# Optimization experiments

Hardware: AMD Instinct MI355X
Metric: run time of the kernel (lower is better)

Reference implementation:

```python
import jax, jax.numpy as jnp
import numpy as np

N, E, IN, HID, H, G, OUT = 50000, 800000, 128, 96, 8, 64, 10
D = HID // H  # per-head dim = 12


def setup_inputs() -> dict:
    key = jax.random.key(0)
    ks = jax.random.split(key, 24)
    s = 0.1
    inp = {
        'x': jax.random.normal(ks[0], (N, IN), jnp.float32),
        'src': jax.random.randint(ks[1], (E,), 0, N, jnp.int32),
        'dst': jax.random.randint(ks[2], (E,), 0, N, jnp.int32),
        'graph_id': jax.random.randint(ks[3], (N,), 0, G, jnp.int32),
        # GraphConv layers (norm='both', weight + bias)
        'W1': jax.random.normal(ks[4], (IN, HID), jnp.float32) * s,
        'b1': jnp.zeros((HID,), jnp.float32),
        'W2': jax.random.normal(ks[5], (HID, HID), jnp.float32) * s,
        'b2': jnp.zeros((HID,), jnp.float32),
        # 3 GATv2 layers, stacked params
        'Ws': jax.random.normal(ks[6], (3, HID, HID), jnp.float32) * s,
        'bs': jnp.zeros((3, HID), jnp.float32),
        'Wd': jax.random.normal(ks[7], (3, HID, HID), jnp.float32) * s,
        'bd': jnp.zeros((3, HID), jnp.float32),
        'attn': jax.random.normal(ks[8], (3, H, D), jnp.float32) * s,
        # classifier MLP (dropout is identity at inference)
        'Wc1': jax.random.normal(ks[9], (HID, HID), jnp.float32) * s,
        'bc1': jnp.zeros((HID,), jnp.float32),
        'Wc2': jax.random.normal(ks[10], (HID, HID // 2), jnp.float32) * s,
        'bc2': jnp.zeros((HID // 2,), jnp.float32),
        'Wc3': jax.random.normal(ks[11], (HID // 2, OUT), jnp.float32) * s,
        'bc3': jnp.zeros((OUT,), jnp.float32),
    }
    return inp


def _graph_conv(h, W, b, src, dst):
    # DGL GraphConv, norm='both', allow_zero_in_degree (degrees clamped to >=1)
    ones = jnp.ones((E,), h.dtype)
    deg_out = jnp.clip(jax.ops.segment_sum(ones, src, N), 1.0)
    deg_in = jnp.clip(jax.ops.segment_sum(ones, dst, N), 1.0)
    h = (h * (deg_out ** -0.5)[:, None]) @ W          # [N, out]
    agg = jax.ops.segment_sum(h[src], dst, N)          # sum over in-edges
    return agg * (deg_in ** -0.5)[:, None] + b


def _gatv2(h, Ws, bs, Wd, bd, attn, src, dst):
    fs = (h @ Ws + bs).reshape(N, H, D)
    fd = (h @ Wd + bd).reshape(N, H, D)
    e = jax.nn.leaky_relu(fs[src] + fd[dst], 0.2)      # [E, H, D]
    logits = jnp.einsum('ehd,hd->eh', e, attn)         # [E, H]
    # edge softmax over incoming edges of each dst node
    m = jax.ops.segment_max(logits, dst, N)            # [N, H]
    ex = jnp.exp(logits - m[dst])
    den = jax.ops.segment_sum(ex, dst, N)              # [N, H]
    a = ex / den[dst]                                  # [E, H]
    rst = jax.ops.segment_sum(a[:, :, None] * fs[src], dst, N)  # [N, H, D]
    return jax.nn.relu(rst).reshape(N, HID)            # activation=relu, then view


def reference(x, src, dst, graph_id, W1, b1, W2, b2, Ws, bs, Wd, bd, attn,
              Wc1, bc1, Wc2, bc2, Wc3, bc3):
    h = jax.nn.relu(_graph_conv(x, W1, b1, src, dst))
    h = jax.nn.relu(_graph_conv(h, W2, b2, src, dst))
    for i in range(3):
        h = _gatv2(h, Ws[i], bs[i], Wd[i], bd[i], attn[i], src, dst)
    # dgl.max_nodes: per-graph max readout
    hg = jax.ops.segment_max(h, graph_id, G)           # [G, HID]
    z = jax.nn.relu(hg @ Wc1 + bc1)
    z = jax.nn.relu(z @ Wc2 + bc2)
    return z @ Wc3 + bc3                               # [G, OUT]
```

## Files before the change

kernel.cpp:

```cpp
#include <hip/hip_runtime.h>
#include <hip/hip_bf16.h>

#define Nn 50000
#define Ee 800000
#define INF_ 128
#define HIDF 96
#define HH 8
#define DD 12
#define GG 64
#define OUTF 10

#define SCAN_CHUNK 512
#define SCAN_BLOCKS ((Nn + SCAN_CHUNK - 1) / SCAN_CHUNK)
#define RB 128

#define HCHK 256
#define HCHKE (Ee / HCHK)
#define NW 12512
#define DBIN 64

__global__ __launch_bounds__(256) void hist_lds(const int* __restrict__ src,
                                                const int* __restrict__ dst,
                                                unsigned int* __restrict__ partS,
                                                unsigned int* __restrict__ partD,
                                                int* __restrict__ edge_slot) {
    __shared__ unsigned int h[NW];
    int b = blockIdx.x, t = threadIdx.x;
    for (int i = t; i < NW; i += 256) h[i] = 0u;
    __syncthreads();
    int base = b * HCHKE;
    for (int i = t; i < HCHKE; i += 256) {
        int d = dst[base + i];
        unsigned int old = atomicAdd(&h[d >> 2], 1u << ((d & 3) * 8));
        edge_slot[base + i] = (int)((old >> ((d & 3) * 8)) & 0xFFu);
    }
    __syncthreads();
    for (int i = t; i < NW; i += 256) { partD[(size_t)b * NW + i] = h[i]; h[i] = 0u; }
    __syncthreads();
    for (int i = t; i < HCHKE; i += 256) {
        int s = src[base + i];
        atomicAdd(&h[s >> 2], 1u << ((s & 3) * 8));
    }
    __syncthreads();
    for (int i = t; i < NW; i += 256) partS[(size_t)b * NW + i] = h[i];
}

__global__ void hist_scan(unsigned int* __restrict__ partD,
                          const unsigned int* __restrict__ partS,
                          int* __restrict__ cnt_in, int* __restrict__ cnt_out) {
    int w = blockIdx.x * 256 + threadIdx.x;
    if (w >= NW) return;
    unsigned int run = 0u, totS = 0u;
    for (int b = 0; b < HCHK; ++b) {
        size_t idx = (size_t)b * NW + w;
        unsigned int v = partD[idx];
        partD[idx] = run;
        run += v;
        totS += partS[idx];
    }
#pragma unroll
    for (int j = 0; j < 4; ++j) {
        int k = w * 4 + j;
        if (k < Nn) {
            cnt_in[k]  = (int)((run >> (j * 8)) & 0xFFu);
            cnt_out[k] = (int)((totS >> (j * 8)) & 0xFFu);
        }
    }
}

__global__ __launch_bounds__(256) void scan1_kernel(const int* __restrict__ cnt_in,
                                                    int* __restrict__ row_start,
                                                    int* __restrict__ blk_sum, int N) {
    __shared__ int part[256];
    int t = threadIdx.x;
    int base = blockIdx.x * SCAN_CHUNK;
    int i0 = base + 2 * t, i1 = i0 + 1;
    int a = (i0 < N) ? cnt_in[i0] : 0;
    int b = (i1 < N) ? cnt_in[i1] : 0;
    int s = a + b;
    part[t] = s;
    __syncthreads();
    for (int off = 1; off < 256; off <<= 1) {
        int v = (t >= off) ? part[t - off] : 0;
        __syncthreads();
        part[t] += v;
        __syncthreads();
    }
    int excl = part[t] - s;
    if (i0 < N) row_start[i0] = excl;
    if (i1 < N) row_start[i1] = excl + a;
    if (t == 255) blk_sum[blockIdx.x] = part[255];
}

__global__ __launch_bounds__(128) void scan2_kernel(const int* __restrict__ blk_sum,
                                                    int* __restrict__ blk_off,
                                                    int* __restrict__ row_start, int N) {
    __shared__ int part[128];
    int t = threadIdx.x;
    int v0 = (t < SCAN_BLOCKS) ? blk_sum[t] : 0;
    part[t] = v0;
    __syncthreads();
    for (int off = 1; off < 128; off <<= 1) {
        int v = (t >= off) ? part[t - off] : 0;
        __syncthreads();
        part[t] += v;
        __syncthreads();
    }
    blk_off[t] = part[t] - v0;
    if (t == 127) row_start[N] = part[127];
}

__global__ __launch_bounds__(256) void scan3_kernel(int* __restrict__ row_start,
                                                    const int* __restrict__ blk_off, int N) {
    int t = threadIdx.x;
    int base = blockIdx.x * SCAN_CHUNK;
    int off = blk_off[blockIdx.x];
    int i0 = base + 2 * t, i1 = i0 + 1;
    if (i0 < N) row_start[i0] += off;
    if (i1 < N) row_start[i1] += off;
}

__global__ void node_setup(const int* __restrict__ cnt_in, const int* __restrict__ cnt_out,
                           float* __restrict__ degI_is, float* __restrict__ degO_is, int N) {
    int n = blockIdx.x * 256 + threadIdx.x;
    if (n < N) {
        degI_is[n] = rsqrtf((float)max(cnt_in[n], 1));
        degO_is[n] = rsqrtf((float)max(cnt_out[n], 1));
    }
}

__global__ __launch_bounds__(256) void fill_kernel(const int* __restrict__ src,
                                                   const int* __restrict__ dst,
                                                   const int* __restrict__ row_start,
                                                   const unsigned int* __restrict__ partD,
                                                   const int* __restrict__ edge_slot,
                                                   int* __restrict__ csr_src) {
    int b = blockIdx.x, t = threadIdx.x;
    int base = b * HCHKE;
    size_t po = (size_t)b * NW;
    for (int i = t; i < HCHKE; i += 256) {
        int e = base + i;
        int d = dst[e];
        int cb = (int)((partD[po + (d >> 2)] >> ((d & 3) * 8)) & 0xFFu);
        csr_src[row_start[d] + cb + edge_slot[e]] = src[e];
    }
}

__global__ __launch_bounds__(256) void deg_hist(const int* __restrict__ cnt_in,
                                                int* __restrict__ dcnt, int N) {
    __shared__ int h[DBIN];
    int t = threadIdx.x;
    if (t < DBIN) h[t] = 0;
    __syncthreads();
    int n = blockIdx.x * 256 + t;
    if (n < N) atomicAdd(&h[DBIN - 1 - min(cnt_in[n], DBIN - 1)], 1);
    __syncthreads();
    if (t < DBIN && h[t]) atomicAdd(&dcnt[t], h[t]);
}

__global__ __launch_bounds__(64) void deg_scan(const int* __restrict__ dcnt,
                                               int* __restrict__ dcur) {
    __shared__ int p[DBIN];
    int t = threadIdx.x;
    int v0 = dcnt[t];
    p[t] = v0;
    __syncthreads();
    for (int o = 1; o < DBIN; o <<= 1) {
        int v = (t >= o) ? p[t - o] : 0;
        __syncthreads();
        p[t] += v;
        __syncthreads();
    }
    dcur[t] = p[t] - v0;
}

__global__ __launch_bounds__(256) void perm_fill(const int* __restrict__ cnt_in,
                                                 int* __restrict__ dcur,
                                                 int* __restrict__ perm, int N) {
    __shared__ int lh[DBIN];
    __shared__ int lbase[DBIN];
    int t = threadIdx.x;
    if (t < DBIN) lh[t] = 0;
    __syncthreads();
    int n = blockIdx.x * 256 + t;
    int bin = 0, lslot = 0;
    if (n < N) {
        bin = DBIN - 1 - min(cnt_in[n], DBIN - 1);
        lslot = atomicAdd(&lh[bin], 1);
    }
    __syncthreads();
    if (t < DBIN) lbase[t] = lh[t] ? atomicAdd(&dcur[t], lh[t]) : 0;
    __syncthreads();
    if (n < N) perm[lbase[bin] + lslot] = n;
}

__global__ __launch_bounds__(192) void gemm96(const float* __restrict__ A, int K,
                                              const float* __restrict__ W,
                                              const float* __restrict__ bias,
                                              const float* __restrict__ rowScale,
                                              float* __restrict__ out, int N) {
    __shared__ float A_lds[64 * 36];
    __shared__ float W_lds[32 * 96];
    const int t = threadIdx.x;
    const int row0 = blockIdx.x * 64;
    const int tcol = t % 24;
    const int trow = t / 24;
    float acc[8][4];
#pragma unroll
    for (int i = 0; i < 8; ++i)
#pragma unroll
        for (int j = 0; j < 4; ++j) acc[i][j] = 0.f;

    for (int k0 = 0; k0 < K; k0 += 32) {
        for (int i = t; i < 32 * 24; i += 192) {
            ((float4*)W_lds)[i] = ((const float4*)W)[(size_t)k0 * 24 + i];
        }
        for (int i = t; i < 64 * 8; i += 192) {
            int r = i / 8, kk = i % 8;
            int gr = row0 + r;
            float4 v = make_float4(0.f, 0.f, 0.f, 0.f);
            if (gr < N) {
                v = *((const float4*)(A + (size_t)gr * K + k0 + kk * 4));
                if (rowScale) {
                    float s = rowScale[gr];
                    v.x *= s; v.y *= s; v.z *= s; v.w *= s;
                }
            }
            *((float4*)(A_lds + r * 36 + kk * 4)) = v;
        }
        __syncthreads();
#pragma unroll
        for (int kk4 = 0; kk4 < 8; ++kk4) {
            float4 a[8];
#pragma unroll
            for (int i = 0; i < 8; ++i)
                a[i] = *((const float4*)(A_lds + (trow + 8 * i) * 36 + kk4 * 4));
#pragma unroll
            for (int kk = 0; kk < 4; ++kk) {
                float4 wv = *((const float4*)(W_lds + (kk4 * 4 + kk) * 96 + tcol * 4));
#pragma unroll
                for (int i = 0; i < 8; ++i) {
                    float av = (kk == 0) ? a[i].x : (kk == 1) ? a[i].y : (kk == 2) ? a[i].z : a[i].w;
                    acc[i][0] = fmaf(av, wv.x, acc[i][0]);
                    acc[i][1] = fmaf(av, wv.y, acc[i][1]);
                    acc[i][2] = fmaf(av, wv.z, acc[i][2]);
                    acc[i][3] = fmaf(av, wv.w, acc[i][3]);
                }
            }
        }
        __syncthreads();
    }
    float4 b4 = bias ? *((const float4*)(bias + tcol * 4)) : make_float4(0.f, 0.f, 0.f, 0.f);
#pragma unroll
    for (int i = 0; i < 8; ++i) {
        int gr = row0 + trow + 8 * i;
        if (gr < N) {
            float4 o = make_float4(acc[i][0] + b4.x, acc[i][1] + b4.y,
                                   acc[i][2] + b4.z, acc[i][3] + b4.w);
            *((float4*)(out + (size_t)gr * 96 + tcol * 4)) = o;
        }
    }
}

__global__ __launch_bounds__(192) void gemm96x2(const float* __restrict__ A,
                                                const float* __restrict__ W1_, const float* __restrict__ b1_,
                                                const float* __restrict__ W2_, const float* __restrict__ b2_,
                                                float* __restrict__ out1, float* __restrict__ out2, int N) {
    __shared__ float A_lds[64 * 36];
    __shared__ float W_lds[2 * 32 * 96];
    const int t = threadIdx.x;
    const int row0 = blockIdx.x * 64;
    const int tcol = t % 24;
    const int trow = t / 24;
    float acc1[8][4], acc2[8][4];
#pragma unroll
    for (int i = 0; i < 8; ++i)
#pragma unroll
        for (int j = 0; j < 4; ++j) { acc1[i][j] = 0.f; acc2[i][j] = 0.f; }

    for (int k0 = 0; k0 < 96; k0 += 32) {
        for (int i = t; i < 32 * 24; i += 192) {
            ((float4*)W_lds)[i] = ((const float4*)W1_)[(size_t)k0 * 24 + i];
            ((float4*)(W_lds + 32 * 96))[i] = ((const float4*)W2_)[(size_t)k0 * 24 + i];
        }
        for (int i = t; i < 64 * 8; i += 192) {
            int r = i / 8, kk = i % 8;
            int gr = row0 + r;
            float4 v = make_float4(0.f, 0.f, 0.f, 0.f);
            if (gr < N) v = *((const float4*)(A + (size_t)gr * 96 + k0 + kk * 4));
            *((float4*)(A_lds + r * 36 + kk * 4)) = v;
        }
        __syncthreads();
#pragma unroll
        for (int kk4 = 0; kk4 < 8; ++kk4) {
            float4 a[8];
#pragma unroll
            for (int i = 0; i < 8; ++i)
                a[i] = *((const float4*)(A_lds + (trow + 8 * i) * 36 + kk4 * 4));
#pragma unroll
            for (int kk = 0; kk < 4; ++kk) {
                float4 wv1 = *((const float4*)(W_lds + (kk4 * 4 + kk) * 96 + tcol * 4));
                float4 wv2 = *((const float4*)(W_lds + 32 * 96 + (kk4 * 4 + kk) * 96 + tcol * 4));
#pragma unroll
                for (int i = 0; i < 8; ++i) {
                    float av = (kk == 0) ? a[i].x : (kk == 1) ? a[i].y : (kk == 2) ? a[i].z : a[i].w;
                    acc1[i][0] = fmaf(av, wv1.x, acc1[i][0]);
                    acc1[i][1] = fmaf(av, wv1.y, acc1[i][1]);
                    acc1[i][2] = fmaf(av, wv1.z, acc1[i][2]);
                    acc1[i][3] = fmaf(av, wv1.w, acc1[i][3]);
                    acc2[i][0] = fmaf(av, wv2.x, acc2[i][0]);
                    acc2[i][1] = fmaf(av, wv2.y, acc2[i][1]);
                    acc2[i][2] = fmaf(av, wv2.z, acc2[i][2]);
                    acc2[i][3] = fmaf(av, wv2.w, acc2[i][3]);
                }
            }
        }
        __syncthreads();
    }
    float4 bb1 = *((const float4*)(b1_ + tcol * 4));
    float4 bb2 = *((const float4*)(b2_ + tcol * 4));
#pragma unroll
    for (int i = 0; i < 8; ++i) {
        int gr = row0 + trow + 8 * i;
        if (gr < N) {
            float4 o1 = make_float4(acc1[i][0] + bb1.x, acc1[i][1] + bb1.y,
                                    acc1[i][2] + bb1.z, acc1[i][3] + bb1.w);
            float4 o2 = make_float4(acc2[i][0] + bb2.x, acc2[i][1] + bb2.y,
                                    acc2[i][2] + bb2.z, acc2[i][3] + bb2.w);
            *((float4*)(out1 + (size_t)gr * 96 + tcol * 4)) = o1;
            *((float4*)(out2 + (size_t)gr * 96 + tcol * 4)) = o2;
        }
    }
}

__global__ __launch_bounds__(192) void gc_agg(const float* __restrict__ hW,
                                              const int* __restrict__ row_start,
                                              const int* __restrict__ csr_src,
                                              const float* __restrict__ degI_is,
                                              const float* __restrict__ bias,
                                              const int* __restrict__ perm,
                                              float* __restrict__ hout, int N) {
    int tid = blockIdx.x * 192 + threadIdx.x;
    int p = tid / 24;
    int c = (tid % 24) * 4;
    if (p >= N) return;
    int n = perm[p];
    int beg = row_start[n], end = row_start[n + 1];
    float4 s = make_float4(0.f, 0.f, 0.f, 0.f);
    int e = beg;
    for (; e + 4 <= end; e += 4) {
        int i0 = csr_src[e], i1 = csr_src[e + 1], i2 = csr_src[e + 2], i3 = csr_src[e + 3];
        float4 v0 = *(const float4*)(hW + (size_t)i0 * 96 + c);
        float4 v1 = *(const float4*)(hW + (size_t)i1 * 96 + c);
        float4 v2 = *(const float4*)(hW + (size_t)i2 * 96 + c);
        float4 v3 = *(const float4*)(hW + (size_t)i3 * 96 + c);
        s.x += (v0.x + v1.x) + (v2.x + v3.x);
        s.y += (v0.y + v1.y) + (v2.y + v3.y);
        s.z += (v0.z + v1.z) + (v2.z + v3.z);
        s.w += (v0.w + v1.w) + (v2.w + v3.w);
    }
    for (; e < end; ++e) {
        int i0 = csr_src[e];
        float4 v0 = *(const float4*)(hW + (size_t)i0 * 96 + c);
        s.x += v0.x; s.y += v0.y; s.z += v0.z; s.w += v0.w;
    }
    float dn = degI_is[n];
    float4 b = *(const float4*)(bias + c);
    float4 o;
    o.x = fmaxf(fmaf(s.x, dn, b.x), 0.f);
    o.y = fmaxf(fmaf(s.y, dn, b.y), 0.f);
    o.z = fmaxf(fmaf(s.z, dn, b.z), 0.f);
    o.w = fmaxf(fmaf(s.w, dn, b.w), 0.f);
    *(float4*)(hout + (size_t)n * 96 + c) = o;
}

__global__ __launch_bounds__(256) void gat_agg(const float* __restrict__ fs,
                                               const float* __restrict__ fd,
                                               const float* __restrict__ attn,
                                               const int* __restrict__ row_start,
                                               const int* __restrict__ csr_src,
                                               const int* __restrict__ perm,
                                               float* __restrict__ hout, int N) {
    int tid = blockIdx.x * 256 + threadIdx.x;
    int p = tid >> 3, hd = tid & 7;
    if (p >= N) return;
    int n = perm[p];
    float att[12], fdv[12];
    {
        const float4* ap = (const float4*)(attn + hd * 12);
        float4 a0 = ap[0], a1 = ap[1], a2 = ap[2];
        att[0]=a0.x; att[1]=a0.y; att[2]=a0.z; att[3]=a0.w;
        att[4]=a1.x; att[5]=a1.y; att[6]=a1.z; att[7]=a1.w;
        att[8]=a2.x; att[9]=a2.y; att[10]=a2.z; att[11]=a2.w;
        const float4* dp = (const float4*)(fd + (size_t)n * 96 + hd * 12);
        float4 d0 = dp[0], d1 = dp[1], d2 = dp[2];
        fdv[0]=d0.x; fdv[1]=d0.y; fdv[2]=d0.z; fdv[3]=d0.w;
        fdv[4]=d1.x; fdv[5]=d1.y; fdv[6]=d1.z; fdv[7]=d1.w;
        fdv[8]=d2.x; fdv[9]=d2.y; fdv[10]=d2.z; fdv[11]=d2.w;
    }
    int beg = row_start[n], end = row_start[n + 1];
    float m0 = -3.0e38f, den0 = 0.f, m1 = -3.0e38f, den1 = 0.f;
    float A0[12], A1[12];
#pragma unroll
    for (int d = 0; d < 12; ++d) { A0[d] = 0.f; A1[d] = 0.f; }

    auto proc = [&](const float4& s0, const float4& s1, const float4& s2,
                    float& m, float& den, float* acc) {
        float fsv[12];
        fsv[0]=s0.x; fsv[1]=s0.y; fsv[2]=s0.z; fsv[3]=s0.w;
        fsv[4]=s1.x; fsv[5]=s1.y; fsv[6]=s1.z; fsv[7]=s1.w;
        fsv[8]=s2.x; fsv[9]=s2.y; fsv[10]=s2.z; fsv[11]=s2.w;
        float logit = 0.f;
#pragma unroll
        for (int d = 0; d < 12; ++d) {
            float u = fsv[d] + fdv[d];
            u = u > 0.f ? u : 0.2f * u;
            logit = fmaf(u, att[d], logit);
        }
        float nm = fmaxf(m, logit);
        float cc = __expf(m - nm);
        float w  = __expf(logit - nm);
        den = fmaf(den, cc, w);
#pragma unroll
        for (int d = 0; d < 12; ++d) acc[d] = fmaf(acc[d], cc, w * fsv[d]);
        m = nm;
    };

    int e = beg;
    for (; e + 4 <= end; e += 4) {
        int i0 = csr_src[e], i1 = csr_src[e + 1], i2 = csr_src[e + 2], i3 = csr_src[e + 3];
        const float4* p0 = (const float4*)(fs + (size_t)i0 * 96 + hd * 12);
        const float4* p1 = (const float4*)(fs + (size_t)i1 * 96 + hd * 12);
        const float4* p2 = (const float4*)(fs + (size_t)i2 * 96 + hd * 12);
        const float4* p3 = (const float4*)(fs + (size_t)i3 * 96 + hd * 12);
        float4 a0 = p0[0], a1 = p0[1], a2 = p0[2];
        float4 b0 = p1[0], b1 = p1[1], b2 = p1[2];
        float4 c0 = p2[0], c1 = p2[1], c2 = p2[2];
        float4 d0 = p3[0], d1 = p3[1], d2 = p3[2];
        proc(a0, a1, a2, m0, den0, A0);
        proc(b0, b1, b2, m1, den1, A1);
        proc(c0, c1, c2, m0, den0, A0);
        proc(d0, d1, d2, m1, den1, A1);
    }
    for (; e < end; ++e) {
        int i0 = csr_src[e];
        const float4* p0 = (const float4*)(fs + (size_t)i0 * 96 + hd * 12);
        float4 a0 = p0[0], a1 = p0[1], a2 = p0[2];
        proc(a0, a1, a2, m0, den0, A0);
    }
    float nm = fmaxf(m0, m1);
    float c0 = __expf(m0 - nm), c1 = __expf(m1 - nm);
    float den = den0 * c0 + den1 * c1;
    float inv = den > 0.f ? 1.f / den : 0.f;
    float* op = hout + (size_t)n * 96 + hd * 12;
#pragma unroll
    for (int d = 0; d < 12; ++d)
        op[d] = fmaxf((A0[d] * c0 + A1[d] * c1) * inv, 0.f);
}

__global__ __launch_bounds__(384) void readout_partial(const float* __restrict__ h,
                                                       const int* __restrict__ graph_id,
                                                       float* __restrict__ partial, int N) {
    __shared__ int lhg[GG * 96];
    int t = threadIdx.x;
    for (int i = t; i < GG * 96; i += 384) lhg[i] = 0;
    __syncthreads();
    int f = t % 96, nl = t / 96;
    for (int n0 = blockIdx.x * 4; n0 < N; n0 += RB * 4) {
        int n = n0 + nl;
        if (n < N) {
            int g = graph_id[n];
            float v = h[(size_t)n * 96 + f];
            atomicMax(&lhg[g * 96 + f], __float_as_int(v));
        }
    }
    __syncthreads();
    for (int i = t; i < GG * 96; i += 384)
        partial[(size_t)blockIdx.x * (GG * 96) + i] = __int_as_float(lhg[i]);
}

__global__ void readout_reduce(const float* __restrict__ partial, float* __restrict__ hg) {
    int i = blockIdx.x * 256 + threadIdx.x;
    if (i < GG * 96) {
        float m = 0.f;
        for (int b = 0; b < RB; ++b) m = fmaxf(m, partial[(size_t)b * (GG * 96) + i]);
        hg[i] = m;
    }
}

__global__ __launch_bounds__(96) void mlp_kernel(const float* __restrict__ hg,
                                                 const float* __restrict__ Wc1, const float* __restrict__ bc1,
                                                 const float* __restrict__ Wc2, const float* __restrict__ bc2,
                                                 const float* __restrict__ Wc3, const float* __restrict__ bc3,
                                                 float* __restrict__ out) {
    int g = blockIdx.x;
    int t = threadIdx.x;
    __shared__ float z0[96], z1[96], z2[48];
    z0[t] = hg[(size_t)g * 96 + t];
    __syncthreads();
    float s = bc1[t];
    for (int k = 0; k < 96; ++k) s = fmaf(z0[k], Wc1[k * 96 + t], s);
    z1[t] = fmaxf(s, 0.f);
    __syncthreads();
    if (t < 48) {
        float s2 = bc2[t];
        for (int k = 0; k < 96; ++k) s2 = fmaf(z1[k], Wc2[k * 48 + t], s2);
        z2[t] = fmaxf(s2, 0.f);
    }
    __syncthreads();
    if (t < 10) {
        float s3 = bc3[t];
        for (int k = 0; k < 48; ++k) s3 = fmaf(z2[k], Wc3[k * 10 + t], s3);
        out[(size_t)g * 10 + t] = s3;
    }
}

extern "C" void kernel_launch(void* const* d_in, const int* in_sizes, int n_in,
                              void* d_out, int out_size, void* d_ws, size_t ws_size,
                              hipStream_t stream) {
    const float* x        = (const float*)d_in[0];
    const int*   src      = (const int*)d_in[1];
    const int*   dst      = (const int*)d_in[2];
    const int*   graph_id = (const int*)d_in[3];
    const float* W1  = (const float*)d_in[4];
    const float* b1  = (const float*)d_in[5];
    const float* W2  = (const float*)d_in[6];
    const float* b2  = (const float*)d_in[7];
    const float* Ws  = (const float*)d_in[8];
    const float* bs  = (const float*)d_in[9];
    const float* Wd  = (const float*)d_in[10];
    const float* bd  = (const float*)d_in[11];
    const float* attn = (const float*)d_in[12];
    const float* Wc1 = (const float*)d_in[13];
    const float* bc1 = (const float*)d_in[14];
    const float* Wc2 = (const float*)d_in[15];
    const float* bc2 = (const float*)d_in[16];
    const float* Wc3 = (const float*)d_in[17];
    const float* bc3 = (const float*)d_in[18];
    float* out = (float*)d_out;

    char* ws = (char*)d_ws;
    size_t off = 0;
    auto alloc = [&](size_t bytes) {
        char* p = ws + off;
        off = (off + bytes + 255) & ~(size_t)255;
        return p;
    };
    int*   cnt_in    = (int*)alloc(Nn * 4);
    int*   cnt_out   = (int*)alloc(Nn * 4);
    int*   row_start = (int*)alloc((Nn + 1) * 4);
    int*   edge_slot = (int*)alloc(Ee * 4);
    int*   csr_src   = (int*)alloc(Ee * 4);
    int*   perm      = (int*)alloc(Nn * 4);
    float* degI_is   = (float*)alloc(Nn * 4);
    float* degO_is   = (float*)alloc(Nn * 4);
    float* bufH      = (float*)alloc((size_t)Nn * 96 * 4);
    float* bufT      = (float*)alloc((size_t)Nn * 96 * 4);
    float* bufFd     = (float*)alloc((size_t)Nn * 96 * 4);
    float* hg        = (float*)alloc(GG * 96 * 4);
    float* partial   = (float*)alloc((size_t)RB * GG * 96 * 4);
    int*   blk_sum   = (int*)alloc(128 * 4);
    int*   blk_off   = (int*)alloc(128 * 4);
    int*   dcnt      = (int*)alloc(DBIN * 4);
    int*   dcur      = (int*)alloc(DBIN * 4);

    unsigned int* partS = (unsigned int*)bufT;
    unsigned int* partD = (unsigned int*)bufFd;

    hipMemsetAsync(dcnt, 0, DBIN * 4, stream);

    hist_lds<<<HCHK, 256, 0, stream>>>(src, dst, partS, partD, edge_slot);
    hist_scan<<<(NW + 255) / 256, 256, 0, stream>>>(partD, partS, cnt_in, cnt_out);
    scan1_kernel<<<SCAN_BLOCKS, 256, 0, stream>>>(cnt_in, row_start, blk_sum, Nn);
    scan2_kernel<<<1, 128, 0, stream>>>(blk_sum, blk_off, row_start, Nn);
    scan3_kernel<<<SCAN_BLOCKS, 256, 0, stream>>>(row_start, blk_off, Nn);
    node_setup<<<(Nn + 255) / 256, 256, 0, stream>>>(cnt_in, cnt_out, degI_is, degO_is, Nn);
    fill_kernel<<<HCHK, 256, 0, stream>>>(src, dst, row_start, partD, edge_slot, csr_src);

    deg_hist<<<(Nn + 255) / 256, 256, 0, stream>>>(cnt_in, dcnt, Nn);
    deg_scan<<<1, 64, 0, stream>>>(dcnt, dcur);
    perm_fill<<<(Nn + 255) / 256, 256, 0, stream>>>(cnt_in, dcur, perm, Nn);

    int gemm_blocks = (Nn + 63) / 64;
    int agg_blocks  = (Nn * 24 + 191) / 192;
    int gat_blocks  = (Nn * 8 + 255) / 256;

    gemm96<<<gemm_blocks, 192, 0, stream>>>(x, 128, W1, nullptr, degO_is, bufT, Nn);
    gc_agg<<<agg_blocks, 192, 0, stream>>>(bufT, row_start, csr_src, degI_is, b1, perm, bufH, Nn);
    gemm96<<<gemm_blocks, 192, 0, stream>>>(bufH, 96, W2, nullptr, degO_is, bufT, Nn);
    gc_agg<<<agg_blocks, 192, 0, stream>>>(bufT, row_start, csr_src, degI_is, b2, perm, bufH, Nn);

    for (int l = 0; l < 3; ++l) {
        const float* Wsl = Ws + (size_t)l * 96 * 96;
        const float* bsl = bs + (size_t)l * 96;
        const float* Wdl = Wd + (size_t)l * 96 * 96;
        const float* bdl = bd + (size_t)l * 96;
        const float* atl = attn + (size_t)l * 96;
        gemm96x2<<<gemm_blocks, 192, 0, stream>>>(bufH, Wsl, bsl, Wdl, bdl, bufT, bufFd, Nn);
        gat_agg<<<gat_blocks, 256, 0, stream>>>(bufT, bufFd, atl, row_start, csr_src, perm, bufH, Nn);
    }

    readout_partial<<<RB, 384, 0, stream>>>(bufH, graph_id, partial, Nn);
    readout_reduce<<<(GG * 96 + 255) / 256, 256, 0, stream>>>(partial, hg);
    mlp_kernel<<<GG, 96, 0, stream>>>(hg, Wc1, bc1, Wc2, bc2, Wc3, bc3, out);
}
```

Baseline: 648.4 us.

## Build CSR via two-pass radix sort so neighbors are src-ordered

Edges are first counting-sorted by source node into a pairs buffer, then counting-sorted stably by destination. Each CSR row therefore lists its source neighbors in ascending order. This should improve cache locality of the feature gathers in the aggregation and attention kernels. The cost is additional histogram, scan and scatter passes over all edges, plus an extra 8-byte-per-edge buffer. Slot arrays are shrunk to bytes.

```diff
diff --git a/kernel.cpp b/kernel.cpp
--- a/kernel.cpp
+++ b/kernel.cpp
@@ -19,64 +19,101 @@
 #define NW 12512
 #define DBIN 64
 
-__global__ __launch_bounds__(256) void hist_lds(const int* __restrict__ src,
-                                                const int* __restrict__ dst,
+__global__ __launch_bounds__(256) void hist_src(const int* __restrict__ src,
                                                 unsigned int* __restrict__ partS,
-                                                unsigned int* __restrict__ partD,
-                                                int* __restrict__ edge_slot) {
+                                                unsigned char* __restrict__ slotS) {
     __shared__ unsigned int h[NW];
     int b = blockIdx.x, t = threadIdx.x;
     for (int i = t; i < NW; i += 256) h[i] = 0u;
     __syncthreads();
     int base = b * HCHKE;
     for (int i = t; i < HCHKE; i += 256) {
-        int d = dst[base + i];
-        unsigned int old = atomicAdd(&h[d >> 2], 1u << ((d & 3) * 8));
-        edge_slot[base + i] = (int)((old >> ((d & 3) * 8)) & 0xFFu);
-    }
-    __syncthreads();
-    for (int i = t; i < NW; i += 256) { partD[(size_t)b * NW + i] = h[i]; h[i] = 0u; }
-    __syncthreads();
-    for (int i = t; i < HCHKE; i += 256) {
         int s = src[base + i];
-        atomicAdd(&h[s >> 2], 1u << ((s & 3) * 8));
+        unsigned int old = atomicAdd(&h[s >> 2], 1u << ((s & 3) * 8));
+        slotS[base + i] = (unsigned char)((old >> ((s & 3) * 8)) & 0xFFu);
     }
     __syncthreads();
     for (int i = t; i < NW; i += 256) partS[(size_t)b * NW + i] = h[i];
 }
 
-__global__ void hist_scan(unsigned int* __restrict__ partD,
-                          const unsigned int* __restrict__ partS,
-                          int* __restrict__ cnt_in, int* __restrict__ cnt_out) {
+__global__ void scan_src(unsigned int* __restrict__ partS, int* __restrict__ cnt_out) {
     int w = blockIdx.x * 256 + threadIdx.x;
     if (w >= NW) return;
-    unsigned int run = 0u, totS = 0u;
+    unsigned int run = 0u;
+    for (int b = 0; b < HCHK; ++b) {
+        size_t idx = (size_t)b * NW + w;
+        unsigned int v = partS[idx];
+        partS[idx] = run;
+        run += v;
+    }
+#pragma unroll
+    for (int j = 0; j < 4; ++j) {
+        int k = w * 4 + j;
+        if (k < Nn) cnt_out[k] = (int)((run >> (j * 8)) & 0xFFu);
+    }
+}
+
+__global__ __launch_bounds__(256) void scatter_edges(const int* __restrict__ src,
+                                                     const int* __restrict__ dst,
+                                                     const int* __restrict__ row_startS,
+                                                     const unsigned int* __restrict__ partS,
+                                                     const unsigned char* __restrict__ slotS,
+                                                     int2* __restrict__ pairs) {
+    int b = blockIdx.x, t = threadIdx.x;
+    int base = b * HCHKE;
+    size_t po = (size_t)b * NW;
+    for (int i = t; i < HCHKE; i += 256) {
+        int e = base + i;
+        int s = src[e];
+        int cb = (int)((partS[po + (s >> 2)] >> ((s & 3) * 8)) & 0xFFu);
+        int pos = row_startS[s] + cb + (int)slotS[e];
+        pairs[pos] = make_int2(s, dst[e]);
+    }
+}
+
+__global__ __launch_bounds__(256) void hist_dst(const int2* __restrict__ pairs,
+                                                unsigned int* __restrict__ partD,
+                                                unsigned char* __restrict__ slotD) {
+    __shared__ unsigned int h[NW];
+    int b = blockIdx.x, t = threadIdx.x;
+    for (int i = t; i < NW; i += 256) h[i] = 0u;
+    __syncthreads();
+    int base = b * HCHKE;
+    for (int i = t; i < HCHKE; i += 256) {
+        int d = pairs[base + i].y;
+        unsigned int old = atomicAdd(&h[d >> 2], 1u << ((d & 3) * 8));
+        slotD[base + i] = (unsigned char)((old >> ((d & 3) * 8)) & 0xFFu);
+    }
+    __syncthreads();
+    for (int i = t; i < NW; i += 256) partD[(size_t)b * NW + i] = h[i];
+}
+
+__global__ void hist_scan(unsigned int* __restrict__ partD, int* __restrict__ cnt_in) {
+    int w = blockIdx.x * 256 + threadIdx.x;
+    if (w >= NW) return;
+    unsigned int run = 0u;
     for (int b = 0; b < HCHK; ++b) {
         size_t idx = (size_t)b * NW + w;
         unsigned int v = partD[idx];
         partD[idx] = run;
         run += v;
-        totS += partS[idx];
     }
 #pragma unroll
     for (int j = 0; j < 4; ++j) {
         int k = w * 4 + j;
-        if (k < Nn) {
-            cnt_in[k]  = (int)((run >> (j * 8)) & 0xFFu);
-            cnt_out[k] = (int)((totS >> (j * 8)) & 0xFFu);
-        }
-    }
-}
-
-__global__ __launch_bounds__(256) void scan1_kernel(const int* __restrict__ cnt_in,
+        if (k < Nn) cnt_in[k] = (int)((run >> (j * 8)) & 0xFFu);
+    }
+}
+
+__global__ __launch_bounds__(256) void scan1_kernel(const int* __restrict__ cnt,
                                                     int* __restrict__ row_start,
                                                     int* __restrict__ blk_sum, int N) {
     __shared__ int part[256];
     int t = threadIdx.x;
     int base = blockIdx.x * SCAN_CHUNK;
     int i0 = base + 2 * t, i1 = i0 + 1;
-    int a = (i0 < N) ? cnt_in[i0] : 0;
-    int b = (i1 < N) ? cnt_in[i1] : 0;
+    int a = (i0 < N) ? cnt[i0] : 0;
+    int b = (i1 < N) ? cnt[i1] : 0;
     int s = a + b;
     part[t] = s;
     __syncthreads();
@@ -129,20 +166,20 @@
     }
 }
 
-__global__ __launch_bounds__(256) void fill_kernel(const int* __restrict__ src,
-                                                   const int* __restrict__ dst,
+__global__ __launch_bounds__(256) void fill_kernel(const int2* __restrict__ pairs,
                                                    const int* __restrict__ row_start,
                                                    const unsigned int* __restrict__ partD,
-                                                   const int* __restrict__ edge_slot,
+                                                   const unsigned char* __restrict__ slotD,
                                                    int* __restrict__ csr_src) {
     int b = blockIdx.x, t = threadIdx.x;
     int base = b * HCHKE;
     size_t po = (size_t)b * NW;
     for (int i = t; i < HCHKE; i += 256) {
         int e = base + i;
-        int d = dst[e];
+        int2 p = pairs[e];
+        int d = p.y;
         int cb = (int)((partD[po + (d >> 2)] >> ((d & 3) * 8)) & 0xFFu);
-        csr_src[row_start[d] + cb + edge_slot[e]] = src[e];
+        csr_src[row_start[d] + cb + (int)slotD[e]] = p.x;
     }
 }
 
@@ -546,36 +583,46 @@
         off = (off + bytes + 255) & ~(size_t)255;
         return p;
     };
-    int*   cnt_in    = (int*)alloc(Nn * 4);
-    int*   cnt_out   = (int*)alloc(Nn * 4);
-    int*   row_start = (int*)alloc((Nn + 1) * 4);
-    int*   edge_slot = (int*)alloc(Ee * 4);
-    int*   csr_src   = (int*)alloc(Ee * 4);
-    int*   perm      = (int*)alloc(Nn * 4);
-    float* degI_is   = (float*)alloc(Nn * 4);
-    float* degO_is   = (float*)alloc(Nn * 4);
-    float* bufH      = (float*)alloc((size_t)Nn * 96 * 4);
-    float* bufT      = (float*)alloc((size_t)Nn * 96 * 4);
-    float* bufFd     = (float*)alloc((size_t)Nn * 96 * 4);
-    float* hg        = (float*)alloc(GG * 96 * 4);
-    float* partial   = (float*)alloc((size_t)RB * GG * 96 * 4);
-    int*   blk_sum   = (int*)alloc(128 * 4);
-    int*   blk_off   = (int*)alloc(128 * 4);
-    int*   dcnt      = (int*)alloc(DBIN * 4);
-    int*   dcur      = (int*)alloc(DBIN * 4);
+    int*   cnt_in     = (int*)alloc(Nn * 4);
+    int*   cnt_out    = (int*)alloc(Nn * 4);
+    int*   row_start  = (int*)alloc((Nn + 1) * 4);
+    int*   row_startS = (int*)alloc((Nn + 1) * 4);
+    unsigned char* slotS = (unsigned char*)alloc(Ee);
+    unsigned char* slotD = (unsigned char*)alloc(Ee);
+    int2*  pairs      = (int2*)alloc((size_t)Ee * 8);
+    int*   csr_src    = (int*)alloc(Ee * 4);
+    int*   perm       = (int*)alloc(Nn * 4);
+    float* degI_is    = (float*)alloc(Nn * 4);
+    float* degO_is    = (float*)alloc(Nn * 4);
+    float* bufH       = (float*)alloc((size_t)Nn * 96 * 4);
+    float* bufT       = (float*)alloc((size_t)Nn * 96 * 4);
+    float* bufFd      = (float*)alloc((size_t)Nn * 96 * 4);
+    float* hg         = (float*)alloc(GG * 96 * 4);
+    float* partial    = (float*)alloc((size_t)RB * GG * 96 * 4);
+    int*   blk_sum    = (int*)alloc(128 * 4);
+    int*   blk_off    = (int*)alloc(128 * 4);
+    int*   dcnt       = (int*)alloc(DBIN * 4);
+    int*   dcur       = (int*)alloc(DBIN * 4);
 
     unsigned int* partS = (unsigned int*)bufT;
     unsigned int* partD = (unsigned int*)bufFd;
 
     hipMemsetAsync(dcnt, 0, DBIN * 4, stream);
 
-    hist_lds<<<HCHK, 256, 0, stream>>>(src, dst, partS, partD, edge_slot);
-    hist_scan<<<(NW + 255) / 256, 256, 0, stream>>>(partD, partS, cnt_in, cnt_out);
+    hist_src<<<HCHK, 256, 0, stream>>>(src, partS, slotS);
+    scan_src<<<(NW + 255) / 256, 256, 0, stream>>>(partS, cnt_out);
+    scan1_kernel<<<SCAN_BLOCKS, 256, 0, stream>>>(cnt_out, row_startS, blk_sum, Nn);
+    scan2_kernel<<<1, 128, 0, stream>>>(blk_sum, blk_off, row_startS, Nn);
+    scan3_kernel<<<SCAN_BLOCKS, 256, 0, stream>>>(row_startS, blk_off, Nn);
+    scatter_edges<<<HCHK, 256, 0, stream>>>(src, dst, row_startS, partS, slotS, pairs);
+
+    hist_dst<<<HCHK, 256, 0, stream>>>(pairs, partD, slotD);
+    hist_scan<<<(NW + 255) / 256, 256, 0, stream>>>(partD, cnt_in);
     scan1_kernel<<<SCAN_BLOCKS, 256, 0, stream>>>(cnt_in, row_start, blk_sum, Nn);
     scan2_kernel<<<1, 128, 0, stream>>>(blk_sum, blk_off, row_start, Nn);
     scan3_kernel<<<SCAN_BLOCKS, 256, 0, stream>>>(row_start, blk_off, Nn);
     node_setup<<<(Nn + 255) / 256, 256, 0, stream>>>(cnt_in, cnt_out, degI_is, degO_is, Nn);
-    fill_kernel<<<HCHK, 256, 0, stream>>>(src, dst, row_start, partD, edge_slot, csr_src);
+    fill_kernel<<<HCHK, 256, 0, stream>>>(pairs, row_start, partD, slotD, csr_src);
 
     deg_hist<<<(Nn + 255) / 256, 256, 0, stream>>>(cnt_in, dcnt, Nn);
     deg_scan<<<1, 64, 0, stream>>>(dcnt, dcur);
```

Measured after the change: 674.1 us. +4.0%, slower.

## Store GEMM outputs head-sliced and split aggregation grids per slice

Applied to the files above, without the earlier changes.

GEMM outputs are now written in a head-major layout, eight slices of [N,12], instead of row-major [N,96]. The GraphConv and GATv2 aggregation kernels are re-gridded so each block handles one slice. Gathers from random source nodes then touch only a 4.8 MB table per slice, which is meant to improve L2/MALL cache hit rates on the irregular loads. The cost is that each source index is now read eight times across blocks, and the GEMM stores become strided.

```diff
diff --git a/kernel.cpp b/kernel.cpp
--- a/kernel.cpp
+++ b/kernel.cpp
@@ -68,15 +68,15 @@
     }
 }
 
-__global__ __launch_bounds__(256) void scan1_kernel(const int* __restrict__ cnt_in,
+__global__ __launch_bounds__(256) void scan1_kernel(const int* __restrict__ cnt,
                                                     int* __restrict__ row_start,
                                                     int* __restrict__ blk_sum, int N) {
     __shared__ int part[256];
     int t = threadIdx.x;
     int base = blockIdx.x * SCAN_CHUNK;
     int i0 = base + 2 * t, i1 = i0 + 1;
-    int a = (i0 < N) ? cnt_in[i0] : 0;
-    int b = (i1 < N) ? cnt_in[i1] : 0;
+    int a = (i0 < N) ? cnt[i0] : 0;
+    int b = (i1 < N) ? cnt[i1] : 0;
     int s = a + b;
     part[t] = s;
     __syncthreads();
@@ -205,6 +205,8 @@
     const int row0 = blockIdx.x * 64;
     const int tcol = t % 24;
     const int trow = t / 24;
+    const int sl = tcol / 3;
+    const int dof = (tcol % 3) * 4;
     float acc[8][4];
 #pragma unroll
     for (int i = 0; i < 8; ++i)
@@ -257,7 +259,7 @@
         if (gr < N) {
             float4 o = make_float4(acc[i][0] + b4.x, acc[i][1] + b4.y,
                                    acc[i][2] + b4.z, acc[i][3] + b4.w);
-            *((float4*)(out + (size_t)gr * 96 + tcol * 4)) = o;
+            *((float4*)(out + (size_t)sl * N * 12 + (size_t)gr * 12 + dof)) = o;
         }
     }
 }
@@ -272,6 +274,8 @@
     const int row0 = blockIdx.x * 64;
     const int tcol = t % 24;
     const int trow = t / 24;
+    const int sl = tcol / 3;
+    const int dof = (tcol % 3) * 4;
     float acc1[8][4], acc2[8][4];
 #pragma unroll
     for (int i = 0; i < 8; ++i)
@@ -327,8 +331,9 @@
                                     acc1[i][2] + bb1.z, acc1[i][3] + bb1.w);
             float4 o2 = make_float4(acc2[i][0] + bb2.x, acc2[i][1] + bb2.y,
                                     acc2[i][2] + bb2.z, acc2[i][3] + bb2.w);
-            *((float4*)(out1 + (size_t)gr * 96 + tcol * 4)) = o1;
-            *((float4*)(out2 + (size_t)gr * 96 + tcol * 4)) = o2;
+            size_t oo = (size_t)sl * N * 12 + (size_t)gr * 12 + dof;
+            *((float4*)(out1 + oo)) = o1;
+            *((float4*)(out2 + oo)) = o2;
         }
     }
 }
@@ -340,20 +345,22 @@
                                               const float* __restrict__ bias,
                                               const int* __restrict__ perm,
                                               float* __restrict__ hout, int N) {
-    int tid = blockIdx.x * 192 + threadIdx.x;
-    int p = tid / 24;
-    int c = (tid % 24) * 4;
+    int sl = blockIdx.x & 7;
+    int t = threadIdx.x;
+    int p = (blockIdx.x >> 3) * 64 + t / 3;
+    int ch = (t % 3) * 4;
     if (p >= N) return;
     int n = perm[p];
+    const float* tab = hW + (size_t)sl * N * 12;
     int beg = row_start[n], end = row_start[n + 1];
     float4 s = make_float4(0.f, 0.f, 0.f, 0.f);
     int e = beg;
     for (; e + 4 <= end; e += 4) {
         int i0 = csr_src[e], i1 = csr_src[e + 1], i2 = csr_src[e + 2], i3 = csr_src[e + 3];
-        float4 v0 = *(const float4*)(hW + (size_t)i0 * 96 + c);
-        float4 v1 = *(const float4*)(hW + (size_t)i1 * 96 + c);
-        float4 v2 = *(const float4*)(hW + (size_t)i2 * 96 + c);
-        float4 v3 = *(const float4*)(hW + (size_t)i3 * 96 + c);
+        float4 v0 = *(const float4*)(tab + (size_t)i0 * 12 + ch);
+        float4 v1 = *(const float4*)(tab + (size_t)i1 * 12 + ch);
+        float4 v2 = *(const float4*)(tab + (size_t)i2 * 12 + ch);
+        float4 v3 = *(const float4*)(tab + (size_t)i3 * 12 + ch);
         s.x += (v0.x + v1.x) + (v2.x + v3.x);
         s.y += (v0.y + v1.y) + (v2.y + v3.y);
         s.z += (v0.z + v1.z) + (v2.z + v3.z);
@@ -361,17 +368,17 @@
     }
     for (; e < end; ++e) {
         int i0 = csr_src[e];
-        float4 v0 = *(const float4*)(hW + (size_t)i0 * 96 + c);
+        float4 v0 = *(const float4*)(tab + (size_t)i0 * 12 + ch);
         s.x += v0.x; s.y += v0.y; s.z += v0.z; s.w += v0.w;
     }
     float dn = degI_is[n];
-    float4 b = *(const float4*)(bias + c);
+    float4 b = *(const float4*)(bias + sl * 12 + ch);
     float4 o;
     o.x = fmaxf(fmaf(s.x, dn, b.x), 0.f);
     o.y = fmaxf(fmaf(s.y, dn, b.y), 0.f);
     o.z = fmaxf(fmaf(s.z, dn, b.z), 0.f);
     o.w = fmaxf(fmaf(s.w, dn, b.w), 0.f);
-    *(float4*)(hout + (size_t)n * 96 + c) = o;
+    *(float4*)(hout + (size_t)n * 96 + sl * 12 + ch) = o;
 }
 
 __global__ __launch_bounds__(256) void gat_agg(const float* __restrict__ fs,
@@ -381,10 +388,11 @@
                                                const int* __restrict__ csr_src,
                                                const int* __restrict__ perm,
                                                float* __restrict__ hout, int N) {
-    int tid = blockIdx.x * 256 + threadIdx.x;
-    int p = tid >> 3, hd = tid & 7;
+    int hd = blockIdx.x & 7;
+    int p = (blockIdx.x >> 3) * 256 + threadIdx.x;
     if (p >= N) return;
     int n = perm[p];
+    const float* tab = fs + (size_t)hd * N * 12;
     float att[12], fdv[12];
     {
         const float4* ap = (const float4*)(attn + hd * 12);
@@ -392,7 +400,7 @@
         att[0]=a0.x; att[1]=a0.y; att[2]=a0.z; att[3]=a0.w;
         att[4]=a1.x; att[5]=a1.y; att[6]=a1.z; att[7]=a1.w;
         att[8]=a2.x; att[9]=a2.y; att[10]=a2.z; att[11]=a2.w;
-        const float4* dp = (const float4*)(fd + (size_t)n * 96 + hd * 12);
+        const float4* dp = (const float4*)(fd + (size_t)hd * N * 12 + (size_t)n * 12);
         float4 d0 = dp[0], d1 = dp[1], d2 = dp[2];
         fdv[0]=d0.x; fdv[1]=d0.y; fdv[2]=d0.z; fdv[3]=d0.w;
         fdv[4]=d1.x; fdv[5]=d1.y; fdv[6]=d1.z; fdv[7]=d1.w;
@@ -429,10 +437,10 @@
     int e = beg;
     for (; e + 4 <= end; e += 4) {
         int i0 = csr_src[e], i1 = csr_src[e + 1], i2 = csr_src[e + 2], i3 = csr_src[e + 3];
-        const float4* p0 = (const float4*)(fs + (size_t)i0 * 96 + hd * 12);
-        const float4* p1 = (const float4*)(fs + (size_t)i1 * 96 + hd * 12);
-        const float4* p2 = (const float4*)(fs + (size_t)i2 * 96 + hd * 12);
-        const float4* p3 = (const float4*)(fs + (size_t)i3 * 96 + hd * 12);
+        const float4* p0 = (const float4*)(tab + (size_t)i0 * 12);
+        const float4* p1 = (const float4*)(tab + (size_t)i1 * 12);
+        const float4* p2 = (const float4*)(tab + (size_t)i2 * 12);
+        const float4* p3 = (const float4*)(tab + (size_t)i3 * 12);
         float4 a0 = p0[0], a1 = p0[1], a2 = p0[2];
         float4 b0 = p1[0], b1 = p1[1], b2 = p1[2];
         float4 c0 = p2[0], c1 = p2[1], c2 = p2[2];
@@ -444,7 +452,7 @@
     }
     for (; e < end; ++e) {
         int i0 = csr_src[e];
-        const float4* p0 = (const float4*)(fs + (size_t)i0 * 96 + hd * 12);
+        const float4* p0 = (const float4*)(tab + (size_t)i0 * 12);
         float4 a0 = p0[0], a1 = p0[1], a2 = p0[2];
         proc(a0, a1, a2, m0, den0, A0);
     }
@@ -582,13 +590,13 @@
     perm_fill<<<(Nn + 255) / 256, 256, 0, stream>>>(cnt_in, dcur, perm, Nn);
 
     int gemm_blocks = (Nn + 63) / 64;
-    int agg_blocks  = (Nn * 24 + 191) / 192;
-    int gat_blocks  = (Nn * 8 + 255) / 256;
+    int gc_blocks   = 8 * ((Nn + 63) / 64);
+    int gat_blocks  = 8 * ((Nn + 255) / 256);
 
     gemm96<<<gemm_blocks, 192, 0, stream>>>(x, 128, W1, nullptr, degO_is, bufT, Nn);
-    gc_agg<<<agg_blocks, 192, 0, stream>>>(bufT, row_start, csr_src, degI_is, b1, perm, bufH, Nn);
+    gc_agg<<<gc_blocks, 192, 0, stream>>>(bufT, row_start, csr_src, degI_is, b1, perm, bufH, Nn);
     gemm96<<<gemm_blocks, 192, 0, stream>>>(bufH, 96, W2, nullptr, degO_is, bufT, Nn);
-    gc_agg<<<agg_blocks, 192, 0, stream>>>(bufT, row_start, csr_src, degI_is, b2, perm, bufH, Nn);
+    gc_agg<<<gc_blocks, 192, 0, stream>>>(bufT, row_start, csr_src, degI_is, b2, perm, bufH, Nn);
 
     for (int l = 0; l < 3; ++l) {
         const float* Wsl = Ws + (size_t)l * 96 * 96;
```

Result: slower. 798.0 us (+23.1%).

## Fuse CSR preprocessing kernels and shrink edge slot storage to bytes

Applied to the files above, without the earlier changes.

Builds src and dst histograms in a single LDS pass with two histograms and 512 threads. Folds degree normalisation and the degree-bin histogram into the histogram scan, and merges the degree-bin scan and perm fill into the existing scan launches. edge_slot becomes a byte array to cut traffic. This reduces kernel launches and memory passes, at the cost of higher LDS usage per block, which lowers occupancy in the histogram kernel.

```diff
diff --git a/kernel.cpp b/kernel.cpp
--- a/kernel.cpp
+++ b/kernel.cpp
@@ -12,6 +12,7 @@
 
 #define SCAN_CHUNK 512
 #define SCAN_BLOCKS ((Nn + SCAN_CHUNK - 1) / SCAN_CHUNK)
+#define NSB ((Nn + 255) / 256)
 #define RB 128
 
 #define HCHK 256
@@ -19,64 +20,77 @@
 #define NW 12512
 #define DBIN 64
 
-__global__ __launch_bounds__(256) void hist_lds(const int* __restrict__ src,
+__global__ __launch_bounds__(512) void hist_lds(const int* __restrict__ src,
                                                 const int* __restrict__ dst,
                                                 unsigned int* __restrict__ partS,
                                                 unsigned int* __restrict__ partD,
-                                                int* __restrict__ edge_slot) {
-    __shared__ unsigned int h[NW];
+                                                unsigned char* __restrict__ edge_slot) {
+    __shared__ unsigned int hS[NW];
+    __shared__ unsigned int hD[NW];
     int b = blockIdx.x, t = threadIdx.x;
-    for (int i = t; i < NW; i += 256) h[i] = 0u;
+    for (int i = t; i < NW; i += 512) { hS[i] = 0u; hD[i] = 0u; }
     __syncthreads();
     int base = b * HCHKE;
-    for (int i = t; i < HCHKE; i += 256) {
+    for (int i = t; i < HCHKE; i += 512) {
         int d = dst[base + i];
-        unsigned int old = atomicAdd(&h[d >> 2], 1u << ((d & 3) * 8));
-        edge_slot[base + i] = (int)((old >> ((d & 3) * 8)) & 0xFFu);
-    }
-    __syncthreads();
-    for (int i = t; i < NW; i += 256) { partD[(size_t)b * NW + i] = h[i]; h[i] = 0u; }
-    __syncthreads();
-    for (int i = t; i < HCHKE; i += 256) {
+        unsigned int old = atomicAdd(&hD[d >> 2], 1u << ((d & 3) * 8));
+        edge_slot[base + i] = (unsigned char)((old >> ((d & 3) * 8)) & 0xFFu);
         int s = src[base + i];
-        atomicAdd(&h[s >> 2], 1u << ((s & 3) * 8));
-    }
-    __syncthreads();
-    for (int i = t; i < NW; i += 256) partS[(size_t)b * NW + i] = h[i];
-}
-
-__global__ void hist_scan(unsigned int* __restrict__ partD,
-                          const unsigned int* __restrict__ partS,
-                          int* __restrict__ cnt_in, int* __restrict__ cnt_out) {
-    int w = blockIdx.x * 256 + threadIdx.x;
-    if (w >= NW) return;
-    unsigned int run = 0u, totS = 0u;
-    for (int b = 0; b < HCHK; ++b) {
-        size_t idx = (size_t)b * NW + w;
-        unsigned int v = partD[idx];
-        partD[idx] = run;
-        run += v;
-        totS += partS[idx];
-    }
-#pragma unroll
-    for (int j = 0; j < 4; ++j) {
-        int k = w * 4 + j;
-        if (k < Nn) {
-            cnt_in[k]  = (int)((run >> (j * 8)) & 0xFFu);
-            cnt_out[k] = (int)((totS >> (j * 8)) & 0xFFu);
-        }
-    }
-}
-
-__global__ __launch_bounds__(256) void scan1_kernel(const int* __restrict__ cnt_in,
+        atomicAdd(&hS[s >> 2], 1u << ((s & 3) * 8));
+    }
+    __syncthreads();
+    for (int i = t; i < NW; i += 512) {
+        partD[(size_t)b * NW + i] = hD[i];
+        partS[(size_t)b * NW + i] = hS[i];
+    }
+}
+
+__global__ __launch_bounds__(256) void hist_scan(unsigned int* __restrict__ partD,
+                                                 const unsigned int* __restrict__ partS,
+                                                 int* __restrict__ cnt_in,
+                                                 float* __restrict__ degI_is,
+                                                 float* __restrict__ degO_is,
+                                                 int* __restrict__ dcnt) {
+    __shared__ int hbin[DBIN];
+    int t = threadIdx.x;
+    if (t < DBIN) hbin[t] = 0;
+    __syncthreads();
+    int w = blockIdx.x * 256 + t;
+    if (w < NW) {
+        unsigned int run = 0u, totS = 0u;
+        for (int b = 0; b < HCHK; ++b) {
+            size_t idx = (size_t)b * NW + w;
+            unsigned int v = partD[idx];
+            partD[idx] = run;
+            run += v;
+            totS += partS[idx];
+        }
+#pragma unroll
+        for (int j = 0; j < 4; ++j) {
+            int k = w * 4 + j;
+            if (k < Nn) {
+                int di = (int)((run >> (j * 8)) & 0xFFu);
+                int dо = (int)((totS >> (j * 8)) & 0xFFu);
+                cnt_in[k] = di;
+                degI_is[k] = rsqrtf((float)max(di, 1));
+                degO_is[k] = rsqrtf((float)max(dо, 1));
+                atomicAdd(&hbin[DBIN - 1 - min(di, DBIN - 1)], 1);
+            }
+        }
+    }
+    __syncthreads();
+    if (t < DBIN && hbin[t]) atomicAdd(&dcnt[t], hbin[t]);
+}
+
+__global__ __launch_bounds__(256) void scan1_kernel(const int* __restrict__ cnt,
                                                     int* __restrict__ row_start,
                                                     int* __restrict__ blk_sum, int N) {
     __shared__ int part[256];
     int t = threadIdx.x;
     int base = blockIdx.x * SCAN_CHUNK;
     int i0 = base + 2 * t, i1 = i0 + 1;
-    int a = (i0 < N) ? cnt_in[i0] : 0;
-    int b = (i1 < N) ? cnt_in[i1] : 0;
+    int a = (i0 < N) ? cnt[i0] : 0;
+    int b = (i1 < N) ? cnt[i1] : 0;
     int s = a + b;
     part[t] = s;
     __syncthreads();
@@ -94,104 +108,82 @@
 
 __global__ __launch_bounds__(128) void scan2_kernel(const int* __restrict__ blk_sum,
                                                     int* __restrict__ blk_off,
-                                                    int* __restrict__ row_start, int N) {
+                                                    int* __restrict__ row_start,
+                                                    const int* __restrict__ dcnt,
+                                                    int* __restrict__ dcur, int N) {
     __shared__ int part[128];
     int t = threadIdx.x;
-    int v0 = (t < SCAN_BLOCKS) ? blk_sum[t] : 0;
-    part[t] = v0;
-    __syncthreads();
-    for (int off = 1; off < 128; off <<= 1) {
-        int v = (t >= off) ? part[t - off] : 0;
-        __syncthreads();
-        part[t] += v;
-        __syncthreads();
-    }
-    blk_off[t] = part[t] - v0;
-    if (t == 127) row_start[N] = part[127];
+    if (blockIdx.x == 0) {
+        int v0 = (t < SCAN_BLOCKS) ? blk_sum[t] : 0;
+        part[t] = v0;
+        __syncthreads();
+        for (int off = 1; off < 128; off <<= 1) {
+            int v = (t >= off) ? part[t - off] : 0;
+            __syncthreads();
+            part[t] += v;
+            __syncthreads();
+        }
+        blk_off[t] = part[t] - v0;
+        if (t == 127) row_start[N] = part[127];
+    } else {
+        int v0 = (t < DBIN) ? dcnt[t] : 0;
+        part[t] = v0;
+        __syncthreads();
+        for (int off = 1; off < DBIN; off <<= 1) {
+            int v = (t >= off) ? part[t - off] : 0;
+            __syncthreads();
+            part[t] += v;
+            __syncthreads();
+        }
+        if (t < DBIN) dcur[t] = part[t] - v0;
+    }
 }
 
 __global__ __launch_bounds__(256) void scan3_kernel(int* __restrict__ row_start,
-                                                    const int* __restrict__ blk_off, int N) {
+                                                    const int* __restrict__ blk_off,
+                                                    const int* __restrict__ cnt_in,
+                                                    int* __restrict__ dcur,
+                                                    int* __restrict__ perm, int N) {
     int t = threadIdx.x;
-    int base = blockIdx.x * SCAN_CHUNK;
-    int off = blk_off[blockIdx.x];
-    int i0 = base + 2 * t, i1 = i0 + 1;
-    if (i0 < N) row_start[i0] += off;
-    if (i1 < N) row_start[i1] += off;
-}
-
-__global__ void node_setup(const int* __restrict__ cnt_in, const int* __restrict__ cnt_out,
-                           float* __restrict__ degI_is, float* __restrict__ degO_is, int N) {
-    int n = blockIdx.x * 256 + threadIdx.x;
-    if (n < N) {
-        degI_is[n] = rsqrtf((float)max(cnt_in[n], 1));
-        degO_is[n] = rsqrtf((float)max(cnt_out[n], 1));
-    }
-}
-
-__global__ __launch_bounds__(256) void fill_kernel(const int* __restrict__ src,
+    if (blockIdx.x < SCAN_BLOCKS) {
+        int base = blockIdx.x * SCAN_CHUNK;
+        int off = blk_off[blockIdx.x];
+        int i0 = base + 2 * t, i1 = i0 + 1;
+        if (i0 < N) row_start[i0] += off;
+        if (i1 < N) row_start[i1] += off;
+    } else {
+        __shared__ int lh[DBIN];
+        __shared__ int lbase[DBIN];
+        if (t < DBIN) lh[t] = 0;
+        __syncthreads();
+        int n = (blockIdx.x - SCAN_BLOCKS) * 256 + t;
+        int bin = 0, lslot = 0;
+        if (n < N) {
+            bin = DBIN - 1 - min(cnt_in[n], DBIN - 1);
+            lslot = atomicAdd(&lh[bin], 1);
+        }
+        __syncthreads();
+        if (t < DBIN) lbase[t] = lh[t] ? atomicAdd(&dcur[t], lh[t]) : 0;
+        __syncthreads();
+        if (n < N) perm[lbase[bin] + lslot] = n;
+    }
+}
+
+__global__ __launch_bounds__(512) void fill_kernel(const int* __restrict__ src,
                                                    const int* __restrict__ dst,
                                                    const int* __restrict__ row_start,
                                                    const unsigned int* __restrict__ partD,
-                                                   const int* __restrict__ edge_slot,
+                                                   const unsigned char* __restrict__ edge_slot,
                                                    int* __restrict__ csr_src) {
     int b = blockIdx.x, t = threadIdx.x;
     int base = b * HCHKE;
     size_t po = (size_t)b * NW;
-    for (int i = t; i < HCHKE; i += 256) {
+    for (int i = t; i < HCHKE; i += 512) {
         int e = base + i;
         int d = dst[e];
         int cb = (int)((partD[po + (d >> 2)] >> ((d & 3) * 8)) & 0xFFu);
-        csr_src[row_start[d] + cb + edge_slot[e]] = src[e];
-    }
-}
-
-__global__ __launch_bounds__(256) void deg_hist(const int* __restrict__ cnt_in,
-                                                int* __restrict__ dcnt, int N) {
-    __shared__ int h[DBIN];
-    int t = threadIdx.x;
-    if (t < DBIN) h[t] = 0;
-    __syncthreads();
-    int n = blockIdx.x * 256 + t;
-    if (n < N) atomicAdd(&h[DBIN - 1 - min(cnt_in[n], DBIN - 1)], 1);
-    __syncthreads();
-    if (t < DBIN && h[t]) atomicAdd(&dcnt[t], h[t]);
-}
-
-__global__ __launch_bounds__(64) void deg_scan(const int* __restrict__ dcnt,
-                                               int* __restrict__ dcur) {
-    __shared__ int p[DBIN];
-    int t = threadIdx.x;
-    int v0 = dcnt[t];
-    p[t] = v0;
-    __syncthreads();
-    for (int o = 1; o < DBIN; o <<= 1) {
-        int v = (t >= o) ? p[t - o] : 0;
-        __syncthreads();
-        p[t] += v;
-        __syncthreads();
-    }
-    dcur[t] = p[t] - v0;
-}
-
-__global__ __launch_bounds__(256) void perm_fill(const int* __restrict__ cnt_in,
-                                                 int* __restrict__ dcur,
-                                                 int* __restrict__ perm, int N) {
-    __shared__ int lh[DBIN];
-    __shared__ int lbase[DBIN];
-    int t = threadIdx.x;
-    if (t < DBIN) lh[t] = 0;
-    __syncthreads();
-    int n = blockIdx.x * 256 + t;
-    int bin = 0, lslot = 0;
-    if (n < N) {
-        bin = DBIN - 1 - min(cnt_in[n], DBIN - 1);
-        lslot = atomicAdd(&lh[bin], 1);
-    }
-    __syncthreads();
-    if (t < DBIN) lbase[t] = lh[t] ? atomicAdd(&dcur[t], lh[t]) : 0;
-    __syncthreads();
-    if (n < N) perm[lbase[bin] + lslot] = n;
+        csr_src[row_start[d] + cb + (int)edge_slot[e]] = src[e];
+    }
 }
 
 __global__ __launch_bounds__(192) void gemm96(const float* __restrict__ A, int K,
@@ -547,9 +539,8 @@
         return p;
     };
     int*   cnt_in    = (int*)alloc(Nn * 4);
-    int*   cnt_out   = (int*)alloc(Nn * 4);
     int*   row_start = (int*)alloc((Nn + 1) * 4);
-    int*   edge_slot = (int*)alloc(Ee * 4);
+    unsigned char* edge_slot = (unsigned char*)alloc(Ee);
     int*   csr_src   = (int*)alloc(Ee * 4);
     int*   perm      = (int*)alloc(Nn * 4);
     float* degI_is   = (float*)alloc(Nn * 4);
@@ -569,17 +560,12 @@
 
     hipMemsetAsync(dcnt, 0, DBIN * 4, stream);
 
-    hist_lds<<<HCHK, 256, 0, stream>>>(src, dst, partS, partD, edge_slot);
-    hist_scan<<<(NW + 255) / 256, 256, 0, stream>>>(partD, partS, cnt_in, cnt_out);
+    hist_lds<<<HCHK, 512, 0, stream>>>(src, dst, partS, partD, edge_slot);
+    hist_scan<<<(NW + 255) / 256, 256, 0, stream>>>(partD, partS, cnt_in, degI_is, degO_is, dcnt);
     scan1_kernel<<<SCAN_BLOCKS, 256, 0, stream>>>(cnt_in, row_start, blk_sum, Nn);
-    scan2_kernel<<<1, 128, 0, stream>>>(blk_sum, blk_off, row_start, Nn);
-    scan3_kernel<<<SCAN_BLOCKS, 256, 0, stream>>>(row_start, blk_off, Nn);
-    node_setup<<<(Nn + 255) / 256, 256, 0, stream>>>(cnt_in, cnt_out, degI_is, degO_is, Nn);
-    fill_kernel<<<HCHK, 256, 0, stream>>>(src, dst, row_start, partD, edge_slot, csr_src);
-
-    deg_hist<<<(Nn + 255) / 256, 256, 0, stream>>>(cnt_in, dcnt, Nn);
-    deg_scan<<<1, 64, 0, stream>>>(dcnt, dcur);
-    perm_fill<<<(Nn + 255) / 256, 256, 0, stream>>>(cnt_in, dcur, perm, Nn);
+    scan2_kernel<<<2, 128, 0, stream>>>(blk_sum, blk_off, row_start, dcnt, dcur, Nn);
+    scan3_kernel<<<SCAN_BLOCKS + NSB, 256, 0, stream>>>(row_start, blk_off, cnt_in, dcur, perm, Nn);
+    fill_kernel<<<HCHK, 512, 0, stream>>>(src, dst, row_start, partD, edge_slot, csr_src);
 
     int gemm_blocks = (Nn + 63) / 64;
     int agg_blocks  = (Nn * 24 + 191) / 192;
```

New measurement: 633.6 us. -2.3%, faster.
